# Kernel optimization log

Hardware: AMD Instinct MI355X
Metric: run time of the kernel (lower is better)

Reference implementation:

```python
import jax, jax.numpy as jnp
import numpy as np

N = 100000   # nodes
E = 3200000  # edges per graph
DP, DA, DF, H, C = 3, 11, 32, 4, 8  # d_p, d_a, d_feat, heads, per-head dim
NEG_SLOPE = 0.2


def gat_conv(x, edge_index, W, att_src, att_dst, bias):
    """PyG GATConv with concat heads and default add_self_loops=True.
    x: [N, DF]; edge_index: [2, E] (row0=src, row1=dst); W: [DF, H*C];
    att_src/att_dst: [H, C]; bias: [H*C]. Returns [N, H*C]."""
    n = x.shape[0]
    loops = jnp.arange(n, dtype=edge_index.dtype)
    src = jnp.concatenate([edge_index[0], loops])
    dst = jnp.concatenate([edge_index[1], loops])
    h = (x @ W).reshape(n, H, C)                       # [N,H,C]
    a_s = jnp.sum(h * att_src[None], axis=-1)          # [N,H]
    a_d = jnp.sum(h * att_dst[None], axis=-1)          # [N,H]
    e = jax.nn.leaky_relu(a_s[src] + a_d[dst], NEG_SLOPE)  # [Etot,H]
    m = jax.ops.segment_max(e, dst, num_segments=n)        # stable softmax per dst
    ex = jnp.exp(e - m[dst])
    den = jax.ops.segment_sum(ex, dst, num_segments=n)
    alpha = ex / den[dst]                               # [Etot,H]
    out = jax.ops.segment_sum(h[src] * alpha[..., None], dst, num_segments=n)
    return out.reshape(n, H * C) + bias


def setup_inputs() -> dict:
    key = jax.random.key(0)
    ks = jax.random.split(key, 32)
    p = lambda k, shp: (jax.random.normal(k, shp, dtype=jnp.float32) * 0.1)
    inp = {
        "F_p_raw": jax.random.normal(ks[0], (N, DP), dtype=jnp.float32),
        "F_a_raw": jax.random.normal(ks[1], (N, DA), dtype=jnp.float32),
        "edge_index_s": jax.random.randint(ks[2], (2, E), 0, N),
        "edge_index_p": jax.random.randint(ks[3], (2, E), 0, N),
        "edge_index_a": jax.random.randint(ks[4], (2, E), 0, N),
        # align linears
        "Wp": p(ks[5], (DP, DF)), "bp": p(ks[6], (DF,)),
        "Wa": p(ks[7], (DA, DF)), "ba": p(ks[8], (DF,)),
        "Ws": p(ks[9], (DP + DA, DF)), "bs": p(ks[10], (DF,)),
        # GAT params per graph
        "Wg_s": p(ks[11], (DF, H * C)), "asrc_s": p(ks[12], (H, C)), "adst_s": p(ks[13], (H, C)), "bg_s": p(ks[14], (H * C,)),
        "Wg_p": p(ks[15], (DF, H * C)), "asrc_p": p(ks[16], (H, C)), "adst_p": p(ks[17], (H, C)), "bg_p": p(ks[18], (H * C,)),
        "Wg_a": p(ks[19], (DF, H * C)), "asrc_a": p(ks[20], (H, C)), "adst_a": p(ks[21], (H, C)), "bg_a": p(ks[22], (H * C,)),
        # fuse MLP
        "W1": p(ks[23], (3 * DF, DF)), "b1": p(ks[24], (DF,)),
        "W2": p(ks[25], (DF, DF)), "b2": p(ks[26], (DF,)),
    }
    return inp


def reference(F_p_raw, F_a_raw, edge_index_s, edge_index_p, edge_index_a,
              Wp, bp, Wa, ba, Ws, bs,
              Wg_s, asrc_s, adst_s, bg_s,
              Wg_p, asrc_p, adst_p, bg_p,
              Wg_a, asrc_a, adst_a, bg_a,
              W1, b1, W2, b2):
    f_s = jnp.concatenate([F_p_raw, F_a_raw], axis=-1) @ Ws + bs
    f_p = F_p_raw @ Wp + bp
    f_a = F_a_raw @ Wa + ba
    h_s = jax.nn.elu(gat_conv(f_s, edge_index_s, Wg_s, asrc_s, adst_s, bg_s))
    h_p = jax.nn.elu(gat_conv(f_p, edge_index_p, Wg_p, asrc_p, adst_p, bg_p))
    h_a = jax.nn.elu(gat_conv(f_a, edge_index_a, Wg_a, asrc_a, adst_a, bg_a))
    h = jnp.concatenate([h_s, h_p, h_a], axis=-1)
    h = jax.nn.relu(h @ W1 + b1)
    return h @ W2 + b2
```

## Files before the change

kernel.cpp:

```cpp
#include <hip/hip_runtime.h>
#include <hip/hip_bf16.h>
#include <stdint.h>

typedef __hip_bfloat16 bf16;

__device__ __forceinline__ float b2f(bf16 v){ return __bfloat162float(v); }

__device__ __forceinline__ uint16_t f2b(float x){
  uint32_t u = __float_as_uint(x);
  return (uint16_t)((u + 0x7FFFu + ((u >> 16) & 1u)) >> 16);
}

__device__ __forceinline__ float loadf(const void* p, int j, bool isb){
  return isb ? b2f(((const bf16*)p)[j]) : ((const float*)p)[j];
}

#define DSTS_PER_BKT 128
#define BKT_SHIFT 7
#define CHUNKE 8192
#define CAP 8192
#define PPT 32
#define BIN_IT 32
#define MAXB 1024
#define NBLKMAX 512
#define ROWS_PER_WAVE (DSTS_PER_BKT / 4)

__global__ __launch_bounds__(256) void k_detect(const void* __restrict__ sample,
                                                int* __restrict__ flag)
{
  __shared__ int bad;
  if (threadIdx.x == 0) bad = 0;
  __syncthreads();
  const unsigned short* u = (const unsigned short*)sample;
  int lbad = 0;
  for (int k = threadIdx.x; k < 1024; k += 256) {
    unsigned short b = u[k];
    unsigned e = (b >> 7) & 0xFFu;
    if (e >= 141u || (e <= 90u && (b & 0x7FFFu) != 0)) lbad = 1;
  }
  if (lbad) atomicOr(&bad, 1);
  __syncthreads();
  if (threadIdx.x == 0) flag[0] = (bad == 0) ? 1 : 0;
}

__global__ __launch_bounds__(256) void k_node(
  const void* __restrict__ rFp, const void* __restrict__ rFa,
  const void* __restrict__ rWp, const void* __restrict__ rbp,
  const void* __restrict__ rWa, const void* __restrict__ rba,
  const void* __restrict__ rWs, const void* __restrict__ rbs,
  const void* __restrict__ rWg0, const void* __restrict__ rAs0, const void* __restrict__ rAd0,
  const void* __restrict__ rWg1, const void* __restrict__ rAs1, const void* __restrict__ rAd1,
  const void* __restrict__ rWg2, const void* __restrict__ rAs2, const void* __restrict__ rAd2,
  const int* __restrict__ flag,
  uint32_t* __restrict__ hgb, uint16_t* __restrict__ asb, float* __restrict__ a_d,
  float* __restrict__ den, float* __restrict__ agg, int N)
{
  __shared__ float sWs[14*32];
  __shared__ float sWp[3*32];
  __shared__ float sWa[11*32];
  __shared__ float sb[3][32];
  __shared__ float sWg[3][32*32];
  __shared__ float sA[3][2][32];
  const int tid = threadIdx.x;
  const bool isb = (*flag) != 0;
  for (int t = tid; t < 14*32; t += 256) sWs[t] = loadf(rWs, t, isb);
  for (int t = tid; t < 3*32;  t += 256) sWp[t] = loadf(rWp, t, isb);
  for (int t = tid; t < 11*32; t += 256) sWa[t] = loadf(rWa, t, isb);
  if (tid < 32) {
    sb[0][tid] = loadf(rbs, tid, isb);
    sb[1][tid] = loadf(rbp, tid, isb);
    sb[2][tid] = loadf(rba, tid, isb);
    sA[0][0][tid] = loadf(rAs0, tid, isb); sA[0][1][tid] = loadf(rAd0, tid, isb);
    sA[1][0][tid] = loadf(rAs1, tid, isb); sA[1][1][tid] = loadf(rAd1, tid, isb);
    sA[2][0][tid] = loadf(rAs2, tid, isb); sA[2][1][tid] = loadf(rAd2, tid, isb);
  }
  for (int t = tid; t < 32*32; t += 256) {
    sWg[0][t] = loadf(rWg0, t, isb);
    sWg[1][t] = loadf(rWg1, t, isb);
    sWg[2][t] = loadf(rWg2, t, isb);
  }
  __syncthreads();

  const int i = blockIdx.x * 256 + tid;
  if (i >= N) return;

  float xp[3], xa[11];
  #pragma unroll
  for (int k = 0; k < 3; ++k)  xp[k] = loadf(rFp, i*3 + k, isb);
  #pragma unroll
  for (int k = 0; k < 11; ++k) xa[k] = loadf(rFa, i*11 + k, isb);

  for (int g = 0; g < 3; ++g) {
    float f[32];
    if (g == 0) {
      #pragma unroll
      for (int j = 0; j < 32; ++j) {
        float acc = sb[0][j];
        #pragma unroll
        for (int k = 0; k < 3; ++k)  acc += xp[k] * sWs[k*32 + j];
        #pragma unroll
        for (int k = 0; k < 11; ++k) acc += xa[k] * sWs[(3+k)*32 + j];
        f[j] = acc;
      }
    } else if (g == 1) {
      #pragma unroll
      for (int j = 0; j < 32; ++j) {
        float acc = sb[1][j];
        #pragma unroll
        for (int k = 0; k < 3; ++k) acc += xp[k] * sWp[k*32 + j];
        f[j] = acc;
      }
    } else {
      #pragma unroll
      for (int j = 0; j < 32; ++j) {
        float acc = sb[2][j];
        #pragma unroll
        for (int k = 0; k < 11; ++k) acc += xa[k] * sWa[k*32 + j];
        f[j] = acc;
      }
    }

    const float* Wg = sWg[g];
    float hv[32];
    #pragma unroll
    for (int j = 0; j < 32; ++j) {
      float acc = 0.f;
      #pragma unroll
      for (int k = 0; k < 32; ++k) acc += f[k] * Wg[k*32 + j];
      hv[j] = acc;
    }

    float asv[4], adv[4], exv[4];
    #pragma unroll
    for (int h = 0; h < 4; ++h) {
      float s0 = 0.f, s1 = 0.f;
      #pragma unroll
      for (int c = 0; c < 8; ++c) {
        s0 += hv[h*8 + c] * sA[g][0][h*8 + c];
        s1 += hv[h*8 + c] * sA[g][1][h*8 + c];
      }
      asv[h] = s0; adv[h] = s1;
      float e = s0 + s1;
      e = e > 0.f ? e : 0.2f * e;
      exv[h] = __expf(e);
    }

    const size_t row = (size_t)g * N + i;
    uint32_t* hp = hgb + row * 16;
    #pragma unroll
    for (int q = 0; q < 4; ++q) {
      uint4 u;
      u.x = (uint32_t)f2b(hv[q*8+0]) | ((uint32_t)f2b(hv[q*8+1]) << 16);
      u.y = (uint32_t)f2b(hv[q*8+2]) | ((uint32_t)f2b(hv[q*8+3]) << 16);
      u.z = (uint32_t)f2b(hv[q*8+4]) | ((uint32_t)f2b(hv[q*8+5]) << 16);
      u.w = (uint32_t)f2b(hv[q*8+6]) | ((uint32_t)f2b(hv[q*8+7]) << 16);
      *(uint4*)(hp + q*4) = u;
    }
    *(ushort4*)(asb + row * 4) =
        make_ushort4(f2b(asv[0]), f2b(asv[1]), f2b(asv[2]), f2b(asv[3]));

    float4* agp = (float4*)(agg + row * 32);
    #pragma unroll
    for (int q = 0; q < 8; ++q) {
      float ex = exv[q >> 1];
      agp[q] = make_float4(ex*hv[q*4+0], ex*hv[q*4+1], ex*hv[q*4+2], ex*hv[q*4+3]);
    }
    *(float4*)(a_d + row*4) = make_float4(adv[0], adv[1], adv[2], adv[3]);
    *(float4*)(den + row*4) = make_float4(exv[0], exv[1], exv[2], exv[3]);
  }
}

__global__ __launch_bounds__(256) void k_bin2(
  const int* __restrict__ ei0, const int* __restrict__ ei1, const int* __restrict__ ei2,
  int* __restrict__ dir, int* __restrict__ bins, int NBPG, int NBLK, int E)
{
  const int g = blockIdx.y;
  const int* __restrict__ ei = (g == 0) ? ei0 : (g == 1 ? ei1 : ei2);
  __shared__ int sp[CHUNKE];
  __shared__ int hist[MAXB];
  __shared__ int soff[MAXB + 1];
  __shared__ int s[256];
  const int tid = threadIdx.x;
  const int blk = blockIdx.x;
  const int base = blk * CHUNKE;
  const int m = min(CHUNKE, E - base);

  for (int t = tid; t < NBPG; t += 256) hist[t] = 0;
  __syncthreads();

  int pk[BIN_IT];
  #pragma unroll
  for (int k = 0; k < BIN_IT; ++k) {
    int idx = base + k * 256 + tid;
    if (idx < E) {
      int d = ei[E + idx];
      int b = d >> BKT_SHIFT;
      int loc = atomicAdd(&hist[b], 1);
      pk[k] = (b << 20) | (loc << 7) | (d & (DSTS_PER_BKT - 1));
    } else pk[k] = -1;
  }
  __syncthreads();

  {
    const int sb = tid * 4;
    int v[4]; int sum = 0;
    #pragma unroll
    for (int j = 0; j < 4; ++j) {
      int i = sb + j; int x = (i < NBPG) ? hist[i] : 0; v[j] = x; sum += x;
    }
    s[tid] = sum;
    __syncthreads();
    for (int d = 1; d < 256; d <<= 1) {
      int t = (tid >= d) ? s[tid - d] : 0;
      __syncthreads();
      s[tid] += t;
      __syncthreads();
    }
    int run = s[tid] - sum;
    #pragma unroll
    for (int j = 0; j < 4; ++j) {
      int i = sb + j;
      if (i < NBPG) { soff[i] = run; run += v[j]; }
    }
    if (tid == 255) soff[NBPG] = s[255];
  }
  __syncthreads();

  for (int t = tid; t <= NBPG; t += 256)
    dir[((size_t)(g * (NBPG + 1) + t)) * NBLK + blk] = soff[t];

  #pragma unroll
  for (int k = 0; k < BIN_IT; ++k) {
    int p = pk[k];
    if (p >= 0) {
      int idx = base + k * 256 + tid;
      int src = ei[idx];
      int b   = p >> 20;
      int loc = (p >> 7) & 0x1FFF;
      int dl  = p & (DSTS_PER_BKT - 1);
      sp[soff[b] + loc] = (dl << 17) | src;
    }
  }
  __syncthreads();

  const size_t ob = ((size_t)(g * NBLK + blk)) << 13;
  for (int i = tid; i < m; i += 256) bins[ob + i] = sp[i];
}

__global__ __launch_bounds__(256, 4) void k_vgather(
  const int* __restrict__ dir, const int* __restrict__ bins,
  const uint32_t* __restrict__ hgb, const uint16_t* __restrict__ asb,
  const float* __restrict__ a_d,
  float* __restrict__ den, float* __restrict__ agg, int NBPG, int NBLK, int N)
{
  __shared__ int sorted[CAP];
  __shared__ int runbase[NBLKMAX];
  __shared__ int pbase[NBLKMAX + 1];
  __shared__ int soff[DSTS_PER_BKT + 1];
  __shared__ int scnt[DSTS_PER_BKT];
  __shared__ int sscan[DSTS_PER_BKT];
  __shared__ int s[256];
  __shared__ int schunk;
  const int g = blockIdx.y, b = blockIdx.x, tid = threadIdx.x;
  const int wave = tid >> 6;
  const int lane = tid & 63;
  const int sub  = lane >> 4;
  const int l16  = lane & 15;
  const int h    = l16 >> 2;
  const size_t gbase = (size_t)g * N;
  const int dst0 = b * DSTS_PER_BKT;

  const int* d0 = dir + ((size_t)(g * (NBPG + 1) + b)) * NBLK;
  const int* d1 = d0 + NBLK;
  for (int t = tid; t < NBLK; t += 256) {
    int r0 = d0[t], r1 = d1[t];
    runbase[t] = ((g * NBLK + t) << 13) + r0;
    pbase[t] = r1 - r0;
  }
  __syncthreads();
  {
    int v0 = (2*tid     < NBLK) ? pbase[2*tid]     : 0;
    int v1 = (2*tid + 1 < NBLK) ? pbase[2*tid + 1] : 0;
    __syncthreads();
    int sum = v0 + v1; s[tid] = sum;
    __syncthreads();
    for (int d = 1; d < 256; d <<= 1) {
      int t = (tid >= d) ? s[tid - d] : 0;
      __syncthreads();
      s[tid] += t;
      __syncthreads();
    }
    int run = s[tid] - sum;
    if (2*tid     <= NBLK) pbase[2*tid]     = run;
    if (2*tid + 1 <= NBLK) pbase[2*tid + 1] = run + v0;
  }
  __syncthreads();
  const int ntot = pbase[NBLK];

  int rlo = 0;
  while (rlo < NBLK) {
    if (tid == 0) {
      if (rlo == 0 && ntot <= CAP) schunk = NBLK;
      else {
        int lim = pbase[rlo] + CAP;
        int hi = rlo + 1;
        while (hi < NBLK && pbase[hi + 1] <= lim) ++hi;
        schunk = hi;
      }
    }
    if (tid < DSTS_PER_BKT) scnt[tid] = 0;
    __syncthreads();
    const int rhi = schunk;
    const int pb0 = pbase[rlo];
    const int m = pbase[rhi] - pb0;

    #pragma unroll 4
    for (int k = 0; k < PPT; ++k) {
      const int j = k * 256 + tid;
      if (j < m) {
        const int j0 = pb0 + j;
        int lo = rlo, hi = rhi;
        while (hi - lo > 1) {
          int mid = (lo + hi) >> 1;
          if (pbase[mid] <= j0) lo = mid; else hi = mid;
        }
        int p = bins[runbase[lo] + (j0 - pbase[lo])];
        sorted[j] = p;
        atomicAdd(&scnt[(p >> 17) & (DSTS_PER_BKT - 1)], 1);
      }
    }
    __syncthreads();
    if (tid < DSTS_PER_BKT) sscan[tid] = scnt[tid];
    __syncthreads();
    for (int d = 1; d < DSTS_PER_BKT; d <<= 1) {
      int t = 0;
      if (tid < DSTS_PER_BKT && tid >= d) t = sscan[tid - d];
      __syncthreads();
      if (tid < DSTS_PER_BKT) sscan[tid] += t;
      __syncthreads();
    }
    if (tid < DSTS_PER_BKT) {
      int ex = sscan[tid] - scnt[tid];
      soff[tid] = ex;
      scnt[tid] = ex;
    }
    if (tid == 0) soff[DSTS_PER_BKT] = m;
    __syncthreads();
    int pv[PPT];
    #pragma unroll
    for (int k = 0; k < PPT; ++k) {
      int i = k * 256 + tid;
      pv[k] = (i < m) ? sorted[i] : -1;
    }
    __syncthreads();
    #pragma unroll
    for (int k = 0; k < PPT; ++k) {
      int p = pv[k];
      if (p >= 0) {
        int pos = atomicAdd(&scnt[(p >> 17) & (DSTS_PER_BKT - 1)], 1);
        sorted[pos] = p & 0x1FFFF;
      }
    }
    __syncthreads();

    const int rbeg = wave * ROWS_PER_WAVE;
    for (int rl = rbeg; rl < rbeg + ROWS_PER_WAVE; ++rl) {
      const int dst = dst0 + rl;
      if (dst >= N) break;
      const int cs = soff[rl], ce = soff[rl + 1];
      const size_t row = gbase + dst;
      const float ad = a_d[row * 4 + h];
      float ax = 0.f, ay = 0.f, w = 0.f;
      for (int c = cs + sub; c < ce; c += 16) {
        const int i0 = c        < ce ? sorted[c]      : -1;
        const int i1 = (c + 4)  < ce ? sorted[c + 4]  : -1;
        const int i2 = (c + 8)  < ce ? sorted[c + 8]  : -1;
        const int i3 = (c + 12) < ce ? sorted[c + 12] : -1;
        const int p0 = i0 < 0 ? 0 : i0;
        const int p1 = i1 < 0 ? 0 : i1;
        const int p2 = i2 < 0 ? 0 : i2;
        const int p3 = i3 < 0 ? 0 : i3;
        const uint32_t u0 = hgb[(gbase + p0) * 16 + l16];
        const uint32_t u1 = hgb[(gbase + p1) * 16 + l16];
        const uint32_t u2 = hgb[(gbase + p2) * 16 + l16];
        const uint32_t u3 = hgb[(gbase + p3) * 16 + l16];
        const uint16_t t0 = asb[(gbase + p0) * 4 + h];
        const uint16_t t1 = asb[(gbase + p1) * 4 + h];
        const uint16_t t2 = asb[(gbase + p2) * 4 + h];
        const uint16_t t3 = asb[(gbase + p3) * 4 + h];
        float e0 = __uint_as_float((uint32_t)t0 << 16) + ad; e0 = e0 > 0.f ? e0 : 0.2f * e0;
        float e1 = __uint_as_float((uint32_t)t1 << 16) + ad; e1 = e1 > 0.f ? e1 : 0.2f * e1;
        float e2 = __uint_as_float((uint32_t)t2 << 16) + ad; e2 = e2 > 0.f ? e2 : 0.2f * e2;
        float e3 = __uint_as_float((uint32_t)t3 << 16) + ad; e3 = e3 > 0.f ? e3 : 0.2f * e3;
        const float w0 = i0 >= 0 ? __expf(e0) : 0.f;
        const float w1 = i1 >= 0 ? __expf(e1) : 0.f;
        const float w2 = i2 >= 0 ? __expf(e2) : 0.f;
        const float w3 = i3 >= 0 ? __expf(e3) : 0.f;
        ax += w0 * __uint_as_float(u0 << 16);
        ay += w0 * __uint_as_float(u0 & 0xFFFF0000u);
        ax += w1 * __uint_as_float(u1 << 16);
        ay += w1 * __uint_as_float(u1 & 0xFFFF0000u);
        ax += w2 * __uint_as_float(u2 << 16);
        ay += w2 * __uint_as_float(u2 & 0xFFFF0000u);
        ax += w3 * __uint_as_float(u3 << 16);
        ay += w3 * __uint_as_float(u3 & 0xFFFF0000u);
        w += w0 + w1 + w2 + w3;
      }
      ax += __shfl_xor(ax, 16); ay += __shfl_xor(ay, 16); w += __shfl_xor(w, 16);
      ax += __shfl_xor(ax, 32); ay += __shfl_xor(ay, 32); w += __shfl_xor(w, 32);
      if (sub == 0) {
        float2* ap = (float2*)(agg + row * 32) + l16;
        float2 sv = *ap;
        sv.x += ax; sv.y += ay;
        *ap = sv;
        if ((l16 & 3) == 0) den[row * 4 + h] += w;
      }
    }
    __syncthreads();
    rlo = rhi;
  }
}

__global__ __launch_bounds__(256) void k_final(
  const float* __restrict__ den, const float* __restrict__ agg,
  const void* __restrict__ rbg0, const void* __restrict__ rbg1, const void* __restrict__ rbg2,
  const void* __restrict__ rW1, const void* __restrict__ rb1,
  const void* __restrict__ rW2, const void* __restrict__ rb2,
  const int* __restrict__ flag, void* __restrict__ out, int N)
{
  __shared__ float sW1[96*32];
  __shared__ float sW2[32*32];
  __shared__ float sb1[32], sb2[32], sbg[3][32];
  const int tid = threadIdx.x;
  const bool isb = (*flag) != 0;
  for (int t = tid; t < 96*32; t += 256) sW1[t] = loadf(rW1, t, isb);
  for (int t = tid; t < 32*32; t += 256) sW2[t] = loadf(rW2, t, isb);
  if (tid < 32) {
    sb1[tid] = loadf(rb1, tid, isb); sb2[tid] = loadf(rb2, tid, isb);
    sbg[0][tid] = loadf(rbg0, tid, isb);
    sbg[1][tid] = loadf(rbg1, tid, isb);
    sbg[2][tid] = loadf(rbg2, tid, isb);
  }
  __syncthreads();

  const int i = blockIdx.x * 256 + tid;
  if (i >= N) return;

  float h96[96];
  #pragma unroll
  for (int g = 0; g < 3; ++g) {
    const size_t row = (size_t)g * N + i;
    float4 d4 = *(const float4*)(den + row * 4);
    float invs[4] = {1.f/d4.x, 1.f/d4.y, 1.f/d4.z, 1.f/d4.w};
    const float4* av = (const float4*)(agg + row * 32);
    #pragma unroll
    for (int q = 0; q < 8; ++q) {
      float4 a4 = av[q];
      float iv = invs[q >> 1];
      float vals[4] = {a4.x, a4.y, a4.z, a4.w};
      #pragma unroll
      for (int k = 0; k < 4; ++k) {
        float v = vals[k] * iv + sbg[g][q*4 + k];
        v = v > 0.f ? v : (__expf(v) - 1.f);
        h96[g*32 + q*4 + k] = v;
      }
    }
  }

  float h1[32];
  #pragma unroll
  for (int j = 0; j < 32; ++j) {
    float acc = sb1[j];
    #pragma unroll
    for (int k = 0; k < 96; ++k) acc += h96[k] * sW1[k*32 + j];
    h1[j] = acc > 0.f ? acc : 0.f;
  }

  #pragma unroll
  for (int j = 0; j < 32; ++j) {
    float acc = sb2[j];
    #pragma unroll
    for (int k = 0; k < 32; ++k) acc += h1[k] * sW2[k*32 + j];
    if (isb) ((bf16*)out)[(size_t)i*32 + j] = __float2bfloat16(acc);
    else     ((float*)out)[(size_t)i*32 + j] = acc;
  }
}

extern "C" void kernel_launch(void* const* d_in, const int* in_sizes, int n_in,
                              void* d_out, int out_size, void* d_ws, size_t ws_size,
                              hipStream_t stream)
{
  const int N = in_sizes[0] / 3;
  const int E = in_sizes[2] / 2;
  const int NBPG = (N + DSTS_PER_BKT - 1) / DSTS_PER_BKT;
  const int NBLK = (E + CHUNKE - 1) / CHUNKE;

  int* flag = (int*)d_ws;
  float* big = (float*)d_ws + 64;
  const size_t n3 = (size_t)3 * N;
  float* agg  = big;
  float* a_d  = agg + n3 * 32;
  float* den  = a_d + n3 * 4;
  uint32_t* hgb = (uint32_t*)(den + n3 * 4);
  uint16_t* asb = (uint16_t*)(hgb + n3 * 16);
  int* dir  = (int*)(asb + n3 * 4);
  int* bins = dir + (size_t)3 * (NBPG + 1) * NBLK;

  k_detect<<<1, 256, 0, stream>>>(d_in[1], flag);
  k_node<<<(N + 255) / 256, 256, 0, stream>>>(
      d_in[0], d_in[1],
      d_in[5], d_in[6], d_in[7], d_in[8], d_in[9], d_in[10],
      d_in[11], d_in[12], d_in[13],
      d_in[15], d_in[16], d_in[17],
      d_in[19], d_in[20], d_in[21],
      flag, hgb, asb, a_d, den, agg, N);

  dim3 gbk((unsigned)NBLK, 3, 1);
  k_bin2<<<gbk, 256, 0, stream>>>(
      (const int*)d_in[2], (const int*)d_in[3], (const int*)d_in[4],
      dir, bins, NBPG, NBLK, E);

  dim3 gg((unsigned)NBPG, 3, 1);
  k_vgather<<<gg, 256, 0, stream>>>(dir, bins, hgb, asb, a_d, den, agg, NBPG, NBLK, N);

  k_final<<<(N + 255) / 256, 256, 0, stream>>>(
      den, agg, d_in[14], d_in[18], d_in[22],
      d_in[23], d_in[24], d_in[25], d_in[26], flag, d_out, N);
}
```

Baseline: 455.4 us.

## Split vgather into source-range passes with XCD-aware graph-to-block mapping

```diff
diff --git a/kernel.cpp b/kernel.cpp
--- a/kernel.cpp
+++ b/kernel.cpp
@@ -251,7 +251,8 @@
   const int* __restrict__ dir, const int* __restrict__ bins,
   const uint32_t* __restrict__ hgb, const uint16_t* __restrict__ asb,
   const float* __restrict__ a_d,
-  float* __restrict__ den, float* __restrict__ agg, int NBPG, int NBLK, int N)
+  float* __restrict__ den, float* __restrict__ agg,
+  int NBPG, int NBLK, int N, int hlo, int hhi)
 {
   __shared__ int sorted[CAP];
   __shared__ int runbase[NBLKMAX];
@@ -261,12 +262,22 @@
   __shared__ int sscan[DSTS_PER_BKT];
   __shared__ int s[256];
   __shared__ int schunk;
-  const int g = blockIdx.y, b = blockIdx.x, tid = threadIdx.x;
+  const int tid = threadIdx.x;
+  const int bid = blockIdx.x;
+  const int xcd = bid & 7, slot = bid >> 3;
+  int g, b;
+  if (xcd < 3)      { g = 0; b = slot * 3 + xcd; }
+  else if (xcd < 6) { g = 1; b = slot * 3 + (xcd - 3); }
+  else              { g = 2; b = slot * 2 + (xcd - 6); }
+  if (b >= NBPG) return;
+
   const int wave = tid >> 6;
   const int lane = tid & 63;
   const int sub  = lane >> 4;
   const int l16  = lane & 15;
   const int h    = l16 >> 2;
+  const int grp16 = tid >> 4;
+  const int ln16  = tid & 15;
   const size_t gbase = (size_t)g * N;
   const int dst0 = b * DSTS_PER_BKT;
 
@@ -314,19 +325,16 @@
     const int pb0 = pbase[rlo];
     const int m = pbase[rhi] - pb0;
 
-    #pragma unroll 4
-    for (int k = 0; k < PPT; ++k) {
-      const int j = k * 256 + tid;
-      if (j < m) {
-        const int j0 = pb0 + j;
-        int lo = rlo, hi = rhi;
-        while (hi - lo > 1) {
-          int mid = (lo + hi) >> 1;
-          if (pbase[mid] <= j0) lo = mid; else hi = mid;
-        }
-        int p = bins[runbase[lo] + (j0 - pbase[lo])];
-        sorted[j] = p;
-        atomicAdd(&scnt[(p >> 17) & (DSTS_PER_BKT - 1)], 1);
+    for (int rr = rlo + grp16; rr < rhi; rr += 16) {
+      const int l = pbase[rr + 1] - pbase[rr];
+      const int gbb = runbase[rr];
+      const int ldst = pbase[rr] - pb0;
+      for (int i = ln16; i < l; i += 16) {
+        int p = bins[gbb + i];
+        sorted[ldst + i] = p;
+        int src = p & 0x1FFFF;
+        if (src >= hlo && src < hhi)
+          atomicAdd(&scnt[(p >> 17) & (DSTS_PER_BKT - 1)], 1);
       }
     }
     __syncthreads();
@@ -343,14 +351,19 @@
       int ex = sscan[tid] - scnt[tid];
       soff[tid] = ex;
       scnt[tid] = ex;
-    }
-    if (tid == 0) soff[DSTS_PER_BKT] = m;
+      if (tid == DSTS_PER_BKT - 1) soff[DSTS_PER_BKT] = sscan[tid];
+    }
     __syncthreads();
     int pv[PPT];
     #pragma unroll
     for (int k = 0; k < PPT; ++k) {
       int i = k * 256 + tid;
-      pv[k] = (i < m) ? sorted[i] : -1;
+      int p = (i < m) ? sorted[i] : -1;
+      if (p >= 0) {
+        int src = p & 0x1FFFF;
+        if (src < hlo || src >= hhi) p = -1;
+      }
+      pv[k] = p;
     }
     __syncthreads();
     #pragma unroll
@@ -494,6 +507,8 @@
   const int E = in_sizes[2] / 2;
   const int NBPG = (N + DSTS_PER_BKT - 1) / DSTS_PER_BKT;
   const int NBLK = (E + CHUNKE - 1) / CHUNKE;
+  const int SLOTS = (NBPG + 1) / 2;
+  const int mid = N >> 1;
 
   int* flag = (int*)d_ws;
   float* big = (float*)d_ws + 64;
@@ -520,8 +535,11 @@
       (const int*)d_in[2], (const int*)d_in[3], (const int*)d_in[4],
       dir, bins, NBPG, NBLK, E);
 
-  dim3 gg((unsigned)NBPG, 3, 1);
-  k_vgather<<<gg, 256, 0, stream>>>(dir, bins, hgb, asb, a_d, den, agg, NBPG, NBLK, N);
+  const unsigned gsz = (unsigned)(8 * SLOTS);
+  k_vgather<<<gsz, 256, 0, stream>>>(dir, bins, hgb, asb, a_d, den, agg,
+                                     NBPG, NBLK, N, 0, mid);
+  k_vgather<<<gsz, 256, 0, stream>>>(dir, bins, hgb, asb, a_d, den, agg,
+                                     NBPG, NBLK, N, mid, N);
 
   k_final<<<(N + 255) / 256, 256, 0, stream>>>(
       den, agg, d_in[14], d_in[18], d_in[22],
```

Result: slower. 695.8 us (+52.8%).
